# Performance work log

Measured on AMD Instinct MI355X. Metric: run time of the kernel, lower is better.

Reference implementation:

```python
import jax, jax.numpy as jnp
import numpy as np

N_NODES = 50000
K_EIG = 512
F_DIM = 128


def setup_inputs() -> dict:
    key = jax.random.key(0)
    k1, k2, k3 = jax.random.split(key, 3)
    eigenvectors = jax.random.normal(k1, (N_NODES, K_EIG), dtype=jnp.float32)
    spectral_filters = jax.random.normal(k2, (K_EIG,), dtype=jnp.float32)
    x = jax.random.normal(k3, (N_NODES, F_DIM), dtype=jnp.float32)
    return {"eigenvectors": eigenvectors, "spectral_filters": spectral_filters, "x": x}


def reference(eigenvectors, spectral_filters, x):
    # U @ diag(g) @ U.T @ x  ==  U @ (g[:, None] * (U.T @ x)); relu epilogue.
    spec = eigenvectors.T @ x                      # [k, f]
    logits = eigenvectors @ (spectral_filters[:, None] * spec)  # [n, f]
    return jax.nn.relu(logits)
```

## Files before the change

### kernel.cpp

```cpp
#include <hip/hip_runtime.h>
#include <hip/hip_bf16.h>

#define N_NODES 50000
#define K_EIG   512
#define F_DIM   128
#define NPAD    51200
#define NSPLITS 200
#define CHUNK   256
#define NT16    3136

typedef __attribute__((ext_vector_type(8))) short bf16x8;
typedef __attribute__((ext_vector_type(4))) short s16x4;
typedef __attribute__((ext_vector_type(4))) float f32x4;
typedef __attribute__((ext_vector_type(2))) unsigned u32x2;

static __device__ __forceinline__ unsigned pk2(float lo, float hi) {
    unsigned short a = __builtin_bit_cast(unsigned short, __float2bfloat16(lo));
    unsigned short b = __builtin_bit_cast(unsigned short, __float2bfloat16(hi));
    return ((unsigned)b << 16) | (unsigned)a;
}

static __device__ __forceinline__ short f2bf(float f) {
    union { float f; unsigned u; } v; v.f = f;
    unsigned r = v.u + 0x7fffu + ((v.u >> 16) & 1u);
    return (short)(r >> 16);
}

static __device__ __forceinline__ float bf2f(unsigned short u) {
    union { unsigned u; float f; } v; v.u = ((unsigned)u) << 16;
    return v.f;
}

__global__ __launch_bounds__(256) void prep_x(const float* __restrict__ x,
                                              unsigned short* __restrict__ xTa)
{
    const int n0 = blockIdx.x * 64;
    const int f0 = blockIdx.y * 64;
    const int fa = threadIdx.x & 15;
    const int nb = threadIdx.x >> 4;
    const int n  = n0 + 4 * nb;
    const int f  = f0 + 4 * fa;

    float r[4][4];
    #pragma unroll
    for (int jj = 0; jj < 4; ++jj) {
        int nr = n + jj;
        if (nr < N_NODES) {
            f32x4 v = *reinterpret_cast<const f32x4*>(x + (long)nr * F_DIM + f);
            r[jj][0] = v[0]; r[jj][1] = v[1]; r[jj][2] = v[2]; r[jj][3] = v[3];
        } else {
            r[jj][0] = r[jj][1] = r[jj][2] = r[jj][3] = 0.f;
        }
    }
    const int nt32 = n >> 5;
    const int hpart = ((n >> 3) & 3) * 16;
    const int slot  = 4 * (nb & 1);
    #pragma unroll
    for (int i = 0; i < 4; ++i) {
        int fi = f + i;
        size_t ad = ((size_t)((fi >> 4) * 1600 + nt32) * 64 + hpart + (fi & 15)) * 8 + slot;
        u32x2 w; w[0] = pk2(r[0][i], r[1][i]); w[1] = pk2(r[2][i], r[3][i]);
        *reinterpret_cast<u32x2*>(xTa + ad) = w;
    }
}

__global__ __launch_bounds__(256) void k_spec_f(
    const float* __restrict__ U, const unsigned short* __restrict__ xTa,
    unsigned short* __restrict__ Ubfa, unsigned short* __restrict__ part2)
{
    __shared__ unsigned char lds1[2][64 * 128];
    __shared__ unsigned char lds2[2][64 * 128];

    const int kt    = blockIdx.x;
    const int split = blockIdx.y;
    const int tid   = threadIdx.x;
    const int wid   = tid >> 6;
    const int lane  = tid & 63;
    const int h     = lane >> 4;
    const int m     = lane & 15;
    const int k0    = kt * 64;
    const int nbeg  = split * CHUNK;

    const int kq = tid & 15;
    const int nq = tid >> 4;

    f32x4 acc[4][2];
    #pragma unroll
    for (int s = 0; s < 4; ++s)
        #pragma unroll
        for (int t = 0; t < 2; ++t)
            #pragma unroll
            for (int e = 0; e < 4; ++e) acc[s][t][e] = 0.f;

    const unsigned short* Bl = xTa + (size_t)lane * 8;
    const int ftb = wid * 2;

    float  r[4][4];
    bf16x8 bfr[2][2];

    #pragma unroll
    for (int j = 0; j < 4; ++j) {
        int n = nbeg + 4 * nq + j;
        if (n < N_NODES) {
            f32x4 v = *reinterpret_cast<const f32x4*>(U + (long)n * K_EIG + k0 + 4 * kq);
            r[j][0] = v[0]; r[j][1] = v[1]; r[j][2] = v[2]; r[j][3] = v[3];
        } else {
            r[j][0] = r[j][1] = r[j][2] = r[j][3] = 0.f;
        }
    }
    #pragma unroll
    for (int sub = 0; sub < 2; ++sub)
        #pragma unroll
        for (int t = 0; t < 2; ++t)
            bfr[sub][t] = *reinterpret_cast<const bf16x8*>(
                Bl + (size_t)((ftb + t) * 1600 + (nbeg >> 5) + sub) * 512);

    #pragma unroll
    for (int step = 0; step < 4; ++step) {
        const int ntile = nbeg + 64 * step;
        const int buf   = step & 1;

        float  rN[4][4];
        bf16x8 bN[2][2];
        if (step < 3) {
            const int nt2 = ntile + 64;
            #pragma unroll
            for (int j = 0; j < 4; ++j) {
                int n = nt2 + 4 * nq + j;
                if (n < N_NODES) {
                    f32x4 v = *reinterpret_cast<const f32x4*>(
                        U + (long)n * K_EIG + k0 + 4 * kq);
                    rN[j][0] = v[0]; rN[j][1] = v[1]; rN[j][2] = v[2]; rN[j][3] = v[3];
                } else {
                    rN[j][0] = rN[j][1] = rN[j][2] = rN[j][3] = 0.f;
                }
            }
            #pragma unroll
            for (int sub = 0; sub < 2; ++sub)
                #pragma unroll
                for (int t = 0; t < 2; ++t)
                    bN[sub][t] = *reinterpret_cast<const bf16x8*>(
                        Bl + (size_t)((ftb + t) * 1600 + (nt2 >> 5) + sub) * 512);
        }

        #pragma unroll
        for (int i = 0; i < 4; ++i) {
            int kl = 4 * kq + i;
            unsigned lo = pk2(r[0][i], r[1][i]);
            unsigned hi = pk2(r[2][i], r[3][i]);
            int byte = (kl * 128 + 8 * nq) ^ ((kl & 7) << 4);
            *reinterpret_cast<unsigned long long*>(&lds1[buf][byte]) =
                ((unsigned long long)hi << 32) | (unsigned long long)lo;
        }
        #pragma unroll
        for (int j = 0; j < 4; ++j) {
            int nl = 4 * nq + j;
            unsigned lo = pk2(r[j][0], r[j][1]);
            unsigned hi = pk2(r[j][2], r[j][3]);
            int byte = (nl * 128 + 8 * kq) ^ ((nl & 7) << 4);
            *reinterpret_cast<unsigned long long*>(&lds2[buf][byte]) =
                ((unsigned long long)hi << 32) | (unsigned long long)lo;
        }
        __syncthreads();

        #pragma unroll
        for (int sub = 0; sub < 2; ++sub) {
            bf16x8 af[4];
            #pragma unroll
            for (int s = 0; s < 4; ++s) {
                int row  = 16 * s + m;
                int byte = (row * 128 + 64 * sub + 16 * h) ^ ((m & 7) << 4);
                af[s] = *reinterpret_cast<const bf16x8*>(&lds1[buf][byte]);
            }
            #pragma unroll
            for (int s = 0; s < 4; ++s)
                #pragma unroll
                for (int t = 0; t < 2; ++t)
                    acc[s][t] = __builtin_amdgcn_mfma_f32_16x16x32_bf16(
                        af[s], bfr[sub][t], acc[s][t], 0, 0, 0);
        }

        {
            const int fid = tid >> 5;
            const int q   = tid & 31;
            const int ntl = fid >> 1;
            const int ktl = fid & 1;
            if (ntile + ntl * 16 < N_NODES) {
                #pragma unroll
                for (int e = 0; e < 2; ++e) {
                    int l    = 2 * q + e;
                    int row  = ntl * 16 + (l & 15);
                    int byte = (row * 128 + ktl * 64 + 16 * (l >> 4)) ^ ((row & 7) << 4);
                    bf16x8 v = *reinterpret_cast<const bf16x8*>(&lds2[buf][byte]);
                    size_t ad = (((size_t)(ntile >> 4) + ntl) * 16 + (kt * 2 + ktl)) * 64 + l;
                    *reinterpret_cast<bf16x8*>(Ubfa + ad * 8) = v;
                }
            }
        }

        if (step < 3) {
            #pragma unroll
            for (int j = 0; j < 4; ++j)
                #pragma unroll
                for (int i = 0; i < 4; ++i) r[j][i] = rN[j][i];
            #pragma unroll
            for (int sub = 0; sub < 2; ++sub)
                #pragma unroll
                for (int t = 0; t < 2; ++t) bfr[sub][t] = bN[sub][t];
        }
    }

    unsigned short* pb = part2 + (((size_t)(kt * NSPLITS + split)) * 256 + tid) * 32;
    #pragma unroll
    for (int s = 0; s < 4; ++s) {
        bf16x8 v;
        #pragma unroll
        for (int e = 0; e < 4; ++e) {
            v[e]     = f2bf(acc[s][0][e]);
            v[e + 4] = f2bf(acc[s][1][e]);
        }
        *reinterpret_cast<bf16x8*>(pb + s * 8) = v;
    }
}

__global__ __launch_bounds__(256) void k_reduce1(
    const unsigned short* __restrict__ part2, float* __restrict__ part3)
{
    const int q  = blockIdx.x * 256 + threadIdx.x;
    const int pg = blockIdx.y;
    const int kt = q >> 11;
    const int tp = (q >> 3) & 255;
    const int sl = q & 7;
    f32x4 s; s[0] = s[1] = s[2] = s[3] = 0.f;
    const int pend = pg * 25 + 25;
    for (int p = pg * 25; p < pend; ++p) {
        s16x4 v = *reinterpret_cast<const s16x4*>(
            part2 + (((size_t)(kt * NSPLITS + p)) * 256 + tp) * 32 + sl * 4);
        s[0] += bf2f((unsigned short)v[0]); s[1] += bf2f((unsigned short)v[1]);
        s[2] += bf2f((unsigned short)v[2]); s[3] += bf2f((unsigned short)v[3]);
    }
    *reinterpret_cast<f32x4*>(part3 + ((size_t)pg * 16384 + q) * 4) = s;
}

__global__ __launch_bounds__(256) void k_reduce2(
    const float* __restrict__ part3, const float* __restrict__ g,
    unsigned short* __restrict__ specbfa)
{
    const int q = blockIdx.x * 256 + threadIdx.x;
    f32x4 s; s[0] = s[1] = s[2] = s[3] = 0.f;
    #pragma unroll
    for (int pg = 0; pg < 8; ++pg) {
        f32x4 v = *reinterpret_cast<const f32x4*>(part3 + ((size_t)pg * 16384 + q) * 4);
        s[0] += v[0]; s[1] += v[1]; s[2] += v[2]; s[3] += v[3];
    }
    const int kt = q >> 11, tp = (q >> 3) & 255, sl = q & 7;
    const int wid = tp >> 6, le = tp & 63, hh = le >> 4, mm = le & 15;
    const int ss = sl >> 1, tt = sl & 1;
    const int f = wid * 32 + tt * 16 + mm;
    const int k = kt * 64 + ss * 16 + hh * 4;
    f32x4 gv = *reinterpret_cast<const f32x4*>(g + k);
    s16x4 o;
    #pragma unroll
    for (int e = 0; e < 4; ++e) o[e] = f2bf(s[e] * gv[e]);
    const int lanep = ((k >> 3) & 3) * 16 + (f & 15);
    size_t ad = ((size_t)((f >> 4) * 16 + (k >> 5)) * 64 + lanep) * 8 + (k & 7);
    *reinterpret_cast<s16x4*>(specbfa + ad) = o;
}

__global__ __launch_bounds__(256) void k_out_bf(
    const unsigned short* __restrict__ Ubfa,
    const unsigned short* __restrict__ specbfa,
    float* __restrict__ out)
{
    const int tid  = threadIdx.x;
    const int wid  = tid >> 6;
    const int lane = tid & 63;
    const int h = lane >> 4, m = lane & 15;
    const int wr = wid >> 1, wc = wid & 1;
    const int nbase = blockIdx.x * 64 + wr * 32;
    const int fbase = wc * 64;

    const unsigned short* Al[2];
    #pragma unroll
    for (int i = 0; i < 2; ++i)
        Al[i] = Ubfa + ((size_t)((nbase >> 4) + i) * 8192 + lane * 8);
    const unsigned short* Blp[4];
    #pragma unroll
    for (int t = 0; t < 4; ++t)
        Blp[t] = specbfa + ((size_t)(4 * wc + t) * 8192 + lane * 8);

    f32x4 acc[2][4];
    #pragma unroll
    for (int i = 0; i < 2; ++i)
        #pragma unroll
        for (int t = 0; t < 4; ++t)
            #pragma unroll
            for (int e = 0; e < 4; ++e) acc[i][t][e] = 0.f;

    bf16x8 aC[2], bC[4];
    #pragma unroll
    for (int i = 0; i < 2; ++i) aC[i] = *reinterpret_cast<const bf16x8*>(Al[i]);
    #pragma unroll
    for (int t = 0; t < 4; ++t) bC[t] = *reinterpret_cast<const bf16x8*>(Blp[t]);

    for (int kb = 0; kb < 16; ++kb) {
        int kn = (kb + 1 < 16) ? kb + 1 : 0;
        bf16x8 aN[2], bN[4];
        #pragma unroll
        for (int i = 0; i < 2; ++i)
            aN[i] = *reinterpret_cast<const bf16x8*>(Al[i] + (size_t)kn * 512);
        #pragma unroll
        for (int t = 0; t < 4; ++t)
            bN[t] = *reinterpret_cast<const bf16x8*>(Blp[t] + (size_t)kn * 512);

        #pragma unroll
        for (int i = 0; i < 2; ++i)
            #pragma unroll
            for (int t = 0; t < 4; ++t)
                acc[i][t] = __builtin_amdgcn_mfma_f32_16x16x32_bf16(
                    aC[i], bC[t], acc[i][t], 0, 0, 0);

        #pragma unroll
        for (int i = 0; i < 2; ++i) aC[i] = aN[i];
        #pragma unroll
        for (int t = 0; t < 4; ++t) bC[t] = bN[t];
    }

    #pragma unroll
    for (int i = 0; i < 2; ++i)
        #pragma unroll
        for (int r = 0; r < 4; ++r) {
            int nn = nbase + 16 * i + 4 * h + r;
            if (nn < N_NODES) {
                float* orow = out + (long)nn * F_DIM + fbase + m;
                #pragma unroll
                for (int t = 0; t < 4; ++t)
                    orow[16 * t] = fmaxf(acc[i][t][r], 0.f);
            }
        }
}

__global__ __launch_bounds__(256) void k_spec_v1(
    const float* __restrict__ U, const float* __restrict__ g,
    const float* __restrict__ x, float* __restrict__ specT)
{
    const int kt    = blockIdx.x;
    const int split = blockIdx.y;
    const int tid   = threadIdx.x;
    const int wid   = tid >> 6;
    const int lane  = tid & 63;
    const int h     = lane >> 4;
    const int m     = lane & 15;
    const int k0 = kt * 64;
    const int f0 = wid * 32;
    const int chunk1 = 782;
    const int n_start = split * chunk1;
    int n_end = n_start + chunk1;
    if (n_end > N_NODES) n_end = N_NODES;

    f32x4 acc[4][2];
    #pragma unroll
    for (int s = 0; s < 4; ++s)
        #pragma unroll
        for (int t = 0; t < 2; ++t)
            #pragma unroll
            for (int e = 0; e < 4; ++e) acc[s][t][e] = 0.f;

    for (int nb = n_start; nb < n_end; nb += 32) {
        bf16x8 a[4]; bf16x8 b[2];
        const int nrow = nb + 8 * h;
        #pragma unroll
        for (int j = 0; j < 8; ++j) {
            int nn = nrow + j;
            bool valid = (nn < n_end);
            int nc = valid ? nn : (n_end - 1);
            const float* Urow = U + (long)nc * K_EIG + k0 + m;
            const float* Xrow = x + (long)nc * F_DIM + f0 + m;
            #pragma unroll
            for (int s = 0; s < 4; ++s) {
                short bv = f2bf(Urow[16 * s]);
                a[s][j] = valid ? bv : (short)0;
            }
            #pragma unroll
            for (int t = 0; t < 2; ++t) {
                short bv = f2bf(Xrow[16 * t]);
                b[t][j] = valid ? bv : (short)0;
            }
        }
        #pragma unroll
        for (int s = 0; s < 4; ++s)
            #pragma unroll
            for (int t = 0; t < 2; ++t)
                acc[s][t] = __builtin_amdgcn_mfma_f32_16x16x32_bf16(
                    a[s], b[t], acc[s][t], 0, 0, 0);
    }
    #pragma unroll
    for (int s = 0; s < 4; ++s)
        #pragma unroll
        for (int t = 0; t < 2; ++t)
            #pragma unroll
            for (int r = 0; r < 4; ++r) {
                int k = k0 + 16 * s + 4 * h + r;
                int f = f0 + 16 * t + m;
                atomicAdd(&specT[(long)f * K_EIG + k], acc[s][t][r] * g[k]);
            }
}

__global__ __launch_bounds__(256) void k_out_v1(
    const float* __restrict__ U, const float* __restrict__ specT,
    float* __restrict__ out)
{
    const int tid  = threadIdx.x;
    const int wid  = tid >> 6;
    const int lane = tid & 63;
    const int h = lane >> 4, m = lane & 15;
    const int wr = wid >> 1, wc = wid & 1;
    const int nbase = blockIdx.x * 128 + wr * 64;
    const int fbase = wc * 64;

    f32x4 acc[4][4];
    #pragma unroll
    for (int i = 0; i < 4; ++i)
        #pragma unroll
        for (int t = 0; t < 4; ++t)
            #pragma unroll
            for (int e = 0; e < 4; ++e) acc[i][t][e] = 0.f;

    for (int kb = 0; kb < K_EIG; kb += 32) {
        bf16x8 a[4], b[4];
        #pragma unroll
        for (int i = 0; i < 4; ++i) {
            int nn = nbase + 16 * i + m;
            bool valid = (nn < N_NODES);
            int nc = valid ? nn : (N_NODES - 1);
            const f32x4* p = reinterpret_cast<const f32x4*>(
                U + (long)nc * K_EIG + kb + 8 * h);
            f32x4 lo = p[0], hi = p[1];
            #pragma unroll
            for (int j = 0; j < 4; ++j) {
                short b0 = f2bf(lo[j]), b1 = f2bf(hi[j]);
                a[i][j]     = valid ? b0 : (short)0;
                a[i][j + 4] = valid ? b1 : (short)0;
            }
        }
        #pragma unroll
        for (int t = 0; t < 4; ++t) {
            const f32x4* p = reinterpret_cast<const f32x4*>(
                specT + (long)(fbase + 16 * t + m) * K_EIG + kb + 8 * h);
            f32x4 lo = p[0], hi = p[1];
            #pragma unroll
            for (int j = 0; j < 4; ++j) {
                b[t][j]     = f2bf(lo[j]);
                b[t][j + 4] = f2bf(hi[j]);
            }
        }
        #pragma unroll
        for (int i = 0; i < 4; ++i)
            #pragma unroll
            for (int t = 0; t < 4; ++t)
                acc[i][t] = __builtin_amdgcn_mfma_f32_16x16x32_bf16(
                    a[i], b[t], acc[i][t], 0, 0, 0);
    }
    #pragma unroll
    for (int i = 0; i < 4; ++i)
        #pragma unroll
        for (int r = 0; r < 4; ++r) {
            int nn = nbase + 16 * i + 4 * h + r;
            if (nn < N_NODES) {
                float* orow = out + (long)nn * F_DIM + fbase + m;
                #pragma unroll
                for (int t = 0; t < 4; ++t)
                    orow[16 * t] = fmaxf(acc[i][t][r], 0.f);
            }
        }
}

extern "C" void kernel_launch(void* const* d_in, const int* in_sizes, int n_in,
                              void* d_out, int out_size, void* d_ws, size_t ws_size,
                              hipStream_t stream) {
    const float* U = (const float*)d_in[0];
    const float* g = (const float*)d_in[1];
    const float* x = (const float*)d_in[2];
    float* out = (float*)d_out;

    const size_t OFF_XTA   = 0;
    const size_t OFF_PART  = 13107200;
    const size_t OFF_SPECA = 39321600;
    const size_t OFF_UBFA  = 39452672;
    const size_t OFF_PART3 = 90832896;
    const size_t WS_NEEDED = 92930048;

    if (ws_size >= WS_NEEDED) {
        unsigned short* xTa     = (unsigned short*)((char*)d_ws + OFF_XTA);
        unsigned short* part2   = (unsigned short*)((char*)d_ws + OFF_PART);
        unsigned short* specbfa = (unsigned short*)((char*)d_ws + OFF_SPECA);
        unsigned short* Ubfa    = (unsigned short*)((char*)d_ws + OFF_UBFA);
        float*          part3   = (float*)((char*)d_ws + OFF_PART3);

        dim3 gx(NPAD / 64, F_DIM / 64);
        prep_x<<<gx, 256, 0, stream>>>(x, xTa);

        dim3 g1(K_EIG / 64, NSPLITS);
        k_spec_f<<<g1, 256, 0, stream>>>(U, xTa, Ubfa, part2);

        dim3 gr1(64, 8);
        k_reduce1<<<gr1, 256, 0, stream>>>(part2, part3);
        k_reduce2<<<64, 256, 0, stream>>>(part3, g, specbfa);

        int nb2 = (N_NODES + 63) / 64;
        k_out_bf<<<nb2, 256, 0, stream>>>(Ubfa, specbfa, out);
    } else {
        float* specT = (float*)d_ws;
        hipMemsetAsync(specT, 0, (size_t)K_EIG * F_DIM * sizeof(float), stream);
        dim3 g1(K_EIG / 64, 64);
        k_spec_v1<<<g1, 256, 0, stream>>>(U, g, x, specT);
        int nb2 = (N_NODES + 127) / 128;
        k_out_v1<<<nb2, 256, 0, stream>>>(U, specT, out);
    }
}
```

Baseline: 95.27 us.

## Split U conversion into separate prep kernel and stream pre-swizzled bf16 tiles in spec GEMM

U is now converted to bf16 by its own kernel, prep_u, which writes two MFMA-ready layouts: a transposed UTa for the first GEMM and Ubfa for the output GEMM. The spec kernel then loads fragments straight from global memory with register double-buffering, so it no longer needs LDS staging or a barrier per step. The split count also changes from 200 to 160 chunks of 320 nodes. In exchange the code writes an extra 52 MB bf16 copy of U and launches one more kernel, and the workspace it needs grows to about 141 MB. If the workspace is smaller than that, the code silently falls back to the slow path.

```diff
diff --git a/kernel.cpp b/kernel.cpp
--- a/kernel.cpp
+++ b/kernel.cpp
@@ -5,9 +5,10 @@
 #define K_EIG   512
 #define F_DIM   128
 #define NPAD    51200
-#define NSPLITS 200
-#define CHUNK   256
-#define NT16    3136
+#define NSPLITS 160
+#define CHUNK   320
+#define NT32    1600
+#define NT16    3200
 
 typedef __attribute__((ext_vector_type(8))) short bf16x8;
 typedef __attribute__((ext_vector_type(4))) short s16x4;
@@ -58,49 +59,29 @@
     #pragma unroll
     for (int i = 0; i < 4; ++i) {
         int fi = f + i;
-        size_t ad = ((size_t)((fi >> 4) * 1600 + nt32) * 64 + hpart + (fi & 15)) * 8 + slot;
+        size_t ad = ((size_t)((fi >> 4) * NT32 + nt32) * 64 + hpart + (fi & 15)) * 8 + slot;
         u32x2 w; w[0] = pk2(r[0][i], r[1][i]); w[1] = pk2(r[2][i], r[3][i]);
         *reinterpret_cast<u32x2*>(xTa + ad) = w;
     }
 }
 
-__global__ __launch_bounds__(256) void k_spec_f(
-    const float* __restrict__ U, const unsigned short* __restrict__ xTa,
-    unsigned short* __restrict__ Ubfa, unsigned short* __restrict__ part2)
-{
-    __shared__ unsigned char lds1[2][64 * 128];
-    __shared__ unsigned char lds2[2][64 * 128];
-
-    const int kt    = blockIdx.x;
-    const int split = blockIdx.y;
-    const int tid   = threadIdx.x;
-    const int wid   = tid >> 6;
-    const int lane  = tid & 63;
-    const int h     = lane >> 4;
-    const int m     = lane & 15;
-    const int k0    = kt * 64;
-    const int nbeg  = split * CHUNK;
-
-    const int kq = tid & 15;
-    const int nq = tid >> 4;
-
-    f32x4 acc[4][2];
-    #pragma unroll
-    for (int s = 0; s < 4; ++s)
-        #pragma unroll
-        for (int t = 0; t < 2; ++t)
-            #pragma unroll
-            for (int e = 0; e < 4; ++e) acc[s][t][e] = 0.f;
-
-    const unsigned short* Bl = xTa + (size_t)lane * 8;
-    const int ftb = wid * 2;
-
-    float  r[4][4];
-    bf16x8 bfr[2][2];
-
+__global__ __launch_bounds__(256) void prep_u(const float* __restrict__ U,
+                                              unsigned short* __restrict__ UTa,
+                                              unsigned short* __restrict__ Ubfa)
+{
+    __shared__ unsigned char lds1[64 * 128];
+    __shared__ unsigned char lds2[64 * 128];
+
+    const int n0  = blockIdx.x * 64;
+    const int k0  = blockIdx.y * 64;
+    const int tid = threadIdx.x;
+    const int kq  = tid & 15;
+    const int nq  = tid >> 4;
+
+    float r[4][4];
     #pragma unroll
     for (int j = 0; j < 4; ++j) {
-        int n = nbeg + 4 * nq + j;
+        int n = n0 + 4 * nq + j;
         if (n < N_NODES) {
             f32x4 v = *reinterpret_cast<const f32x4*>(U + (long)n * K_EIG + k0 + 4 * kq);
             r[j][0] = v[0]; r[j][1] = v[1]; r[j][2] = v[2]; r[j][3] = v[3];
@@ -108,109 +89,112 @@
             r[j][0] = r[j][1] = r[j][2] = r[j][3] = 0.f;
         }
     }
-    #pragma unroll
-    for (int sub = 0; sub < 2; ++sub)
+
+    #pragma unroll
+    for (int i = 0; i < 4; ++i) {
+        int kl = 4 * kq + i;
+        unsigned lo = pk2(r[0][i], r[1][i]);
+        unsigned hi = pk2(r[2][i], r[3][i]);
+        int byte = (kl * 128 + 8 * nq) ^ ((kl & 7) << 4);
+        *reinterpret_cast<unsigned long long*>(lds1 + byte) =
+            ((unsigned long long)hi << 32) | (unsigned long long)lo;
+    }
+    #pragma unroll
+    for (int j = 0; j < 4; ++j) {
+        int nl = 4 * nq + j;
+        unsigned lo = pk2(r[j][0], r[j][1]);
+        unsigned hi = pk2(r[j][2], r[j][3]);
+        int byte = (nl * 128 + 8 * kq) ^ ((nl & 7) << 4);
+        *reinterpret_cast<unsigned long long*>(lds2 + byte) =
+            ((unsigned long long)hi << 32) | (unsigned long long)lo;
+    }
+    __syncthreads();
+
+    const int q = tid & 31;
+    {
+        const int fid = tid >> 5;
+        const int ntl = fid >> 1;
+        const int ktl = fid & 1;
+        #pragma unroll
+        for (int e = 0; e < 2; ++e) {
+            int l    = 2 * q + e;
+            int row  = ntl * 16 + (l & 15);
+            int byte = (row * 128 + ktl * 64 + 16 * (l >> 4)) ^ ((row & 7) << 4);
+            bf16x8 v = *reinterpret_cast<const bf16x8*>(lds2 + byte);
+            size_t ad = (((size_t)(n0 >> 4) + ntl) * 16 + ((k0 >> 5) + ktl)) * 64 + l;
+            *reinterpret_cast<bf16x8*>(Ubfa + ad * 8) = v;
+        }
+    }
+    {
+        const int fid = tid >> 5;
+        const int ktl = fid >> 1;
+        const int ntl = fid & 1;
+        #pragma unroll
+        for (int e = 0; e < 2; ++e) {
+            int l    = 2 * q + e;
+            int row  = ktl * 16 + (l & 15);
+            int byte = (row * 128 + ntl * 64 + 16 * (l >> 4)) ^ ((row & 7) << 4);
+            bf16x8 v = *reinterpret_cast<const bf16x8*>(lds1 + byte);
+            size_t ad = (((size_t)(k0 >> 4) + ktl) * NT32 + ((n0 >> 5) + ntl)) * 64 + l;
+            *reinterpret_cast<bf16x8*>(UTa + ad * 8) = v;
+        }
+    }
+}
+
+__global__ __launch_bounds__(256) void k_spec(
+    const unsigned short* __restrict__ UTa, const unsigned short* __restrict__ xTa,
+    unsigned short* __restrict__ part2)
+{
+    const int ktB   = blockIdx.x;
+    const int split = blockIdx.y;
+    const int tid   = threadIdx.x;
+    const int wid   = tid >> 6;
+    const int lane  = tid & 63;
+    const int nt0   = split * (CHUNK / 32);
+
+    f32x4 acc[4][2];
+    #pragma unroll
+    for (int s = 0; s < 4; ++s)
         #pragma unroll
         for (int t = 0; t < 2; ++t)
-            bfr[sub][t] = *reinterpret_cast<const bf16x8*>(
-                Bl + (size_t)((ftb + t) * 1600 + (nbeg >> 5) + sub) * 512);
-
-    #pragma unroll
-    for (int step = 0; step < 4; ++step) {
-        const int ntile = nbeg + 64 * step;
-        const int buf   = step & 1;
-
-        float  rN[4][4];
-        bf16x8 bN[2][2];
-        if (step < 3) {
-            const int nt2 = ntile + 64;
-            #pragma unroll
-            for (int j = 0; j < 4; ++j) {
-                int n = nt2 + 4 * nq + j;
-                if (n < N_NODES) {
-                    f32x4 v = *reinterpret_cast<const f32x4*>(
-                        U + (long)n * K_EIG + k0 + 4 * kq);
-                    rN[j][0] = v[0]; rN[j][1] = v[1]; rN[j][2] = v[2]; rN[j][3] = v[3];
-                } else {
-                    rN[j][0] = rN[j][1] = rN[j][2] = rN[j][3] = 0.f;
-                }
-            }
-            #pragma unroll
-            for (int sub = 0; sub < 2; ++sub)
-                #pragma unroll
-                for (int t = 0; t < 2; ++t)
-                    bN[sub][t] = *reinterpret_cast<const bf16x8*>(
-                        Bl + (size_t)((ftb + t) * 1600 + (nt2 >> 5) + sub) * 512);
-        }
-
-        #pragma unroll
-        for (int i = 0; i < 4; ++i) {
-            int kl = 4 * kq + i;
-            unsigned lo = pk2(r[0][i], r[1][i]);
-            unsigned hi = pk2(r[2][i], r[3][i]);
-            int byte = (kl * 128 + 8 * nq) ^ ((kl & 7) << 4);
-            *reinterpret_cast<unsigned long long*>(&lds1[buf][byte]) =
-                ((unsigned long long)hi << 32) | (unsigned long long)lo;
-        }
-        #pragma unroll
-        for (int j = 0; j < 4; ++j) {
-            int nl = 4 * nq + j;
-            unsigned lo = pk2(r[j][0], r[j][1]);
-            unsigned hi = pk2(r[j][2], r[j][3]);
-            int byte = (nl * 128 + 8 * kq) ^ ((nl & 7) << 4);
-            *reinterpret_cast<unsigned long long*>(&lds2[buf][byte]) =
-                ((unsigned long long)hi << 32) | (unsigned long long)lo;
-        }
-        __syncthreads();
-
-        #pragma unroll
-        for (int sub = 0; sub < 2; ++sub) {
-            bf16x8 af[4];
-            #pragma unroll
-            for (int s = 0; s < 4; ++s) {
-                int row  = 16 * s + m;
-                int byte = (row * 128 + 64 * sub + 16 * h) ^ ((m & 7) << 4);
-                af[s] = *reinterpret_cast<const bf16x8*>(&lds1[buf][byte]);
-            }
-            #pragma unroll
-            for (int s = 0; s < 4; ++s)
-                #pragma unroll
-                for (int t = 0; t < 2; ++t)
-                    acc[s][t] = __builtin_amdgcn_mfma_f32_16x16x32_bf16(
-                        af[s], bfr[sub][t], acc[s][t], 0, 0, 0);
-        }
-
-        {
-            const int fid = tid >> 5;
-            const int q   = tid & 31;
-            const int ntl = fid >> 1;
-            const int ktl = fid & 1;
-            if (ntile + ntl * 16 < N_NODES) {
-                #pragma unroll
-                for (int e = 0; e < 2; ++e) {
-                    int l    = 2 * q + e;
-                    int row  = ntl * 16 + (l & 15);
-                    int byte = (row * 128 + ktl * 64 + 16 * (l >> 4)) ^ ((row & 7) << 4);
-                    bf16x8 v = *reinterpret_cast<const bf16x8*>(&lds2[buf][byte]);
-                    size_t ad = (((size_t)(ntile >> 4) + ntl) * 16 + (kt * 2 + ktl)) * 64 + l;
-                    *reinterpret_cast<bf16x8*>(Ubfa + ad * 8) = v;
-                }
-            }
-        }
-
-        if (step < 3) {
-            #pragma unroll
-            for (int j = 0; j < 4; ++j)
-                #pragma unroll
-                for (int i = 0; i < 4; ++i) r[j][i] = rN[j][i];
-            #pragma unroll
-            for (int sub = 0; sub < 2; ++sub)
-                #pragma unroll
-                for (int t = 0; t < 2; ++t) bfr[sub][t] = bN[sub][t];
-        }
-    }
-
-    unsigned short* pb = part2 + (((size_t)(kt * NSPLITS + split)) * 256 + tid) * 32;
+            #pragma unroll
+            for (int e = 0; e < 4; ++e) acc[s][t][e] = 0.f;
+
+    const unsigned short* Abase = UTa + ((size_t)(ktB * 4) * NT32) * 512 + lane * 8;
+    const unsigned short* Bbase = xTa + ((size_t)(wid * 2) * NT32) * 512 + lane * 8;
+
+    bf16x8 aC[4], bC[2];
+    #pragma unroll
+    for (int s = 0; s < 4; ++s)
+        aC[s] = *reinterpret_cast<const bf16x8*>(Abase + ((size_t)s * NT32 + nt0) * 512);
+    #pragma unroll
+    for (int t = 0; t < 2; ++t)
+        bC[t] = *reinterpret_cast<const bf16x8*>(Bbase + ((size_t)t * NT32 + nt0) * 512);
+
+    for (int step = 0; step < CHUNK / 32; ++step) {
+        int ntn = nt0 + ((step + 1 < CHUNK / 32) ? step + 1 : 0);
+        bf16x8 aN[4], bN[2];
+        #pragma unroll
+        for (int s = 0; s < 4; ++s)
+            aN[s] = *reinterpret_cast<const bf16x8*>(Abase + ((size_t)s * NT32 + ntn) * 512);
+        #pragma unroll
+        for (int t = 0; t < 2; ++t)
+            bN[t] = *reinterpret_cast<const bf16x8*>(Bbase + ((size_t)t * NT32 + ntn) * 512);
+
+        #pragma unroll
+        for (int s = 0; s < 4; ++s)
+            #pragma unroll
+            for (int t = 0; t < 2; ++t)
+                acc[s][t] = __builtin_amdgcn_mfma_f32_16x16x32_bf16(
+                    aC[s], bC[t], acc[s][t], 0, 0, 0);
+
+        #pragma unroll
+        for (int s = 0; s < 4; ++s) aC[s] = aN[s];
+        #pragma unroll
+        for (int t = 0; t < 2; ++t) bC[t] = bN[t];
+    }
+
+    unsigned short* pb = part2 + (((size_t)(ktB * NSPLITS + split)) * 256 + tid) * 32;
     #pragma unroll
     for (int s = 0; s < 4; ++s) {
         bf16x8 v;
@@ -232,8 +216,8 @@
     const int tp = (q >> 3) & 255;
     const int sl = q & 7;
     f32x4 s; s[0] = s[1] = s[2] = s[3] = 0.f;
-    const int pend = pg * 25 + 25;
-    for (int p = pg * 25; p < pend; ++p) {
+    const int pend = pg * 20 + 20;
+    for (int p = pg * 20; p < pend; ++p) {
         s16x4 v = *reinterpret_cast<const s16x4*>(
             part2 + (((size_t)(kt * NSPLITS + p)) * 256 + tp) * 32 + sl * 4);
         s[0] += bf2f((unsigned short)v[0]); s[1] += bf2f((unsigned short)v[1]);
@@ -484,24 +468,29 @@
     float* out = (float*)d_out;
 
     const size_t OFF_XTA   = 0;
-    const size_t OFF_PART  = 13107200;
-    const size_t OFF_SPECA = 39321600;
-    const size_t OFF_UBFA  = 39452672;
-    const size_t OFF_PART3 = 90832896;
-    const size_t WS_NEEDED = 92930048;
+    const size_t OFF_UTA   = 13107200;
+    const size_t OFF_UBFA  = 65536000;
+    const size_t OFF_PART2 = 117964800;
+    const size_t OFF_PART3 = 138936320;
+    const size_t OFF_SPECA = 141033472;
+    const size_t WS_NEEDED = 141164544;
 
     if (ws_size >= WS_NEEDED) {
         unsigned short* xTa     = (unsigned short*)((char*)d_ws + OFF_XTA);
-        unsigned short* part2   = (unsigned short*)((char*)d_ws + OFF_PART);
+        unsigned short* UTa     = (unsigned short*)((char*)d_ws + OFF_UTA);
+        unsigned short* Ubfa    = (unsigned short*)((char*)d_ws + OFF_UBFA);
+        unsigned short* part2   = (unsigned short*)((char*)d_ws + OFF_PART2);
+        float*          part3   = (float*)((char*)d_ws + OFF_PART3);
         unsigned short* specbfa = (unsigned short*)((char*)d_ws + OFF_SPECA);
-        unsigned short* Ubfa    = (unsigned short*)((char*)d_ws + OFF_UBFA);
-        float*          part3   = (float*)((char*)d_ws + OFF_PART3);
 
         dim3 gx(NPAD / 64, F_DIM / 64);
         prep_x<<<gx, 256, 0, stream>>>(x, xTa);
 
+        dim3 gu(NPAD / 64, K_EIG / 64);
+        prep_u<<<gu, 256, 0, stream>>>(U, UTa, Ubfa);
+
         dim3 g1(K_EIG / 64, NSPLITS);
-        k_spec_f<<<g1, 256, 0, stream>>>(U, xTa, Ubfa, part2);
+        k_spec<<<g1, 256, 0, stream>>>(UTa, xTa, part2);
 
         dim3 gr1(64, 8);
         k_reduce1<<<gr1, 256, 0, stream>>>(part2, part3);
```

Result: slower. 107.1 us (+12.5%).

## Drop bf16 eigenvector staging; read fp32 U directly in output GEMM

Applied to the files above, without the earlier changes.

The first GEMM no longer writes a bf16 copy of U (Ubfa) through a second LDS transpose buffer. The output GEMM now loads fp32 rows of U directly and converts them to bf16 in registers before each MFMA. This removes a ~51MB write and a 51MB read of the bf16 copy, at the cost of reading 102MB of fp32 U in the second pass and doing conversion ALU work there. The spec-kernel grid order is also swapped so the split index is blockIdx.x.

```diff
diff --git a/kernel.cpp b/kernel.cpp
--- a/kernel.cpp
+++ b/kernel.cpp
@@ -7,7 +7,7 @@
 #define NPAD    51200
 #define NSPLITS 200
 #define CHUNK   256
-#define NT16    3136
+#define NT32    1600
 
 typedef __attribute__((ext_vector_type(8))) short bf16x8;
 typedef __attribute__((ext_vector_type(4))) short s16x4;
@@ -58,7 +58,7 @@
     #pragma unroll
     for (int i = 0; i < 4; ++i) {
         int fi = f + i;
-        size_t ad = ((size_t)((fi >> 4) * 1600 + nt32) * 64 + hpart + (fi & 15)) * 8 + slot;
+        size_t ad = ((size_t)((fi >> 4) * NT32 + nt32) * 64 + hpart + (fi & 15)) * 8 + slot;
         u32x2 w; w[0] = pk2(r[0][i], r[1][i]); w[1] = pk2(r[2][i], r[3][i]);
         *reinterpret_cast<u32x2*>(xTa + ad) = w;
     }
@@ -66,13 +66,12 @@
 
 __global__ __launch_bounds__(256) void k_spec_f(
     const float* __restrict__ U, const unsigned short* __restrict__ xTa,
-    unsigned short* __restrict__ Ubfa, unsigned short* __restrict__ part2)
+    unsigned short* __restrict__ part2)
 {
     __shared__ unsigned char lds1[2][64 * 128];
-    __shared__ unsigned char lds2[2][64 * 128];
-
-    const int kt    = blockIdx.x;
-    const int split = blockIdx.y;
+
+    const int split = blockIdx.x;
+    const int kt    = blockIdx.y;
     const int tid   = threadIdx.x;
     const int wid   = tid >> 6;
     const int lane  = tid & 63;
@@ -113,7 +112,7 @@
         #pragma unroll
         for (int t = 0; t < 2; ++t)
             bfr[sub][t] = *reinterpret_cast<const bf16x8*>(
-                Bl + (size_t)((ftb + t) * 1600 + (nbeg >> 5) + sub) * 512);
+                Bl + (size_t)((ftb + t) * NT32 + (nbeg >> 5) + sub) * 512);
 
     #pragma unroll
     for (int step = 0; step < 4; ++step) {
@@ -140,7 +139,7 @@
                 #pragma unroll
                 for (int t = 0; t < 2; ++t)
                     bN[sub][t] = *reinterpret_cast<const bf16x8*>(
-                        Bl + (size_t)((ftb + t) * 1600 + (nt2 >> 5) + sub) * 512);
+                        Bl + (size_t)((ftb + t) * NT32 + (nt2 >> 5) + sub) * 512);
         }
 
         #pragma unroll
@@ -152,15 +151,6 @@
             *reinterpret_cast<unsigned long long*>(&lds1[buf][byte]) =
                 ((unsigned long long)hi << 32) | (unsigned long long)lo;
         }
-        #pragma unroll
-        for (int j = 0; j < 4; ++j) {
-            int nl = 4 * nq + j;
-            unsigned lo = pk2(r[j][0], r[j][1]);
-            unsigned hi = pk2(r[j][2], r[j][3]);
-            int byte = (nl * 128 + 8 * kq) ^ ((nl & 7) << 4);
-            *reinterpret_cast<unsigned long long*>(&lds2[buf][byte]) =
-                ((unsigned long long)hi << 32) | (unsigned long long)lo;
-        }
         __syncthreads();
 
         #pragma unroll
@@ -178,24 +168,6 @@
                 for (int t = 0; t < 2; ++t)
                     acc[s][t] = __builtin_amdgcn_mfma_f32_16x16x32_bf16(
                         af[s], bfr[sub][t], acc[s][t], 0, 0, 0);
-        }
-
-        {
-            const int fid = tid >> 5;
-            const int q   = tid & 31;
-            const int ntl = fid >> 1;
-            const int ktl = fid & 1;
-            if (ntile + ntl * 16 < N_NODES) {
-                #pragma unroll
-                for (int e = 0; e < 2; ++e) {
-                    int l    = 2 * q + e;
-                    int row  = ntl * 16 + (l & 15);
-                    int byte = (row * 128 + ktl * 64 + 16 * (l >> 4)) ^ ((row & 7) << 4);
-                    bf16x8 v = *reinterpret_cast<const bf16x8*>(&lds2[buf][byte]);
-                    size_t ad = (((size_t)(ntile >> 4) + ntl) * 16 + (kt * 2 + ktl)) * 64 + l;
-                    *reinterpret_cast<bf16x8*>(Ubfa + ad * 8) = v;
-                }
-            }
         }
 
         if (step < 3) {
@@ -267,9 +239,8 @@
     *reinterpret_cast<s16x4*>(specbfa + ad) = o;
 }
 
-__global__ __launch_bounds__(256) void k_out_bf(
-    const unsigned short* __restrict__ Ubfa,
-    const unsigned short* __restrict__ specbfa,
+__global__ __launch_bounds__(256) void k_out_f32(
+    const float* __restrict__ U, const unsigned short* __restrict__ specbfa,
     float* __restrict__ out)
 {
     const int tid  = threadIdx.x;
@@ -280,10 +251,13 @@
     const int nbase = blockIdx.x * 64 + wr * 32;
     const int fbase = wc * 64;
 
-    const unsigned short* Al[2];
-    #pragma unroll
-    for (int i = 0; i < 2; ++i)
-        Al[i] = Ubfa + ((size_t)((nbase >> 4) + i) * 8192 + lane * 8);
+    const float* Arow[2];
+    #pragma unroll
+    for (int i = 0; i < 2; ++i) {
+        int n  = nbase + 16 * i + m;
+        int nc = (n < N_NODES) ? n : (N_NODES - 1);
+        Arow[i] = U + (size_t)nc * K_EIG + 8 * h;
+    }
     const unsigned short* Blp[4];
     #pragma unroll
     for (int t = 0; t < 4; ++t)
@@ -297,31 +271,45 @@
             #pragma unroll
             for (int e = 0; e < 4; ++e) acc[i][t][e] = 0.f;
 
-    bf16x8 aC[2], bC[4];
-    #pragma unroll
-    for (int i = 0; i < 2; ++i) aC[i] = *reinterpret_cast<const bf16x8*>(Al[i]);
-    #pragma unroll
-    for (int t = 0; t < 4; ++t) bC[t] = *reinterpret_cast<const bf16x8*>(Blp[t]);
+    f32x4 loC[2], hiC[2]; bf16x8 bC[4];
+    #pragma unroll
+    for (int i = 0; i < 2; ++i) {
+        loC[i] = *reinterpret_cast<const f32x4*>(Arow[i]);
+        hiC[i] = *reinterpret_cast<const f32x4*>(Arow[i] + 4);
+    }
+    #pragma unroll
+    for (int t = 0; t < 4; ++t)
+        bC[t] = *reinterpret_cast<const bf16x8*>(Blp[t]);
 
     for (int kb = 0; kb < 16; ++kb) {
         int kn = (kb + 1 < 16) ? kb + 1 : 0;
-        bf16x8 aN[2], bN[4];
-        #pragma unroll
-        for (int i = 0; i < 2; ++i)
-            aN[i] = *reinterpret_cast<const bf16x8*>(Al[i] + (size_t)kn * 512);
+        f32x4 loN[2], hiN[2]; bf16x8 bN[4];
+        #pragma unroll
+        for (int i = 0; i < 2; ++i) {
+            loN[i] = *reinterpret_cast<const f32x4*>(Arow[i] + kn * 32);
+            hiN[i] = *reinterpret_cast<const f32x4*>(Arow[i] + kn * 32 + 4);
+        }
         #pragma unroll
         for (int t = 0; t < 4; ++t)
             bN[t] = *reinterpret_cast<const bf16x8*>(Blp[t] + (size_t)kn * 512);
 
+        bf16x8 a[2];
+        #pragma unroll
+        for (int i = 0; i < 2; ++i)
+            #pragma unroll
+            for (int j = 0; j < 4; ++j) {
+                a[i][j]     = f2bf(loC[i][j]);
+                a[i][j + 4] = f2bf(hiC[i][j]);
+            }
         #pragma unroll
         for (int i = 0; i < 2; ++i)
             #pragma unroll
             for (int t = 0; t < 4; ++t)
                 acc[i][t] = __builtin_amdgcn_mfma_f32_16x16x32_bf16(
-                    aC[i], bC[t], acc[i][t], 0, 0, 0);
-
-        #pragma unroll
-        for (int i = 0; i < 2; ++i) aC[i] = aN[i];
+                    a[i], bC[t], acc[i][t], 0, 0, 0);
+
+        #pragma unroll
+        for (int i = 0; i < 2; ++i) { loC[i] = loN[i]; hiC[i] = hiN[i]; }
         #pragma unroll
         for (int t = 0; t < 4; ++t) bC[t] = bN[t];
     }
@@ -484,31 +472,29 @@
     float* out = (float*)d_out;
 
     const size_t OFF_XTA   = 0;
-    const size_t OFF_PART  = 13107200;
-    const size_t OFF_SPECA = 39321600;
-    const size_t OFF_UBFA  = 39452672;
-    const size_t OFF_PART3 = 90832896;
-    const size_t WS_NEEDED = 92930048;
+    const size_t OFF_PART2 = 13107200;
+    const size_t OFF_PART3 = 39321600;
+    const size_t OFF_SPECA = 41418752;
+    const size_t WS_NEEDED = 41549824;
 
     if (ws_size >= WS_NEEDED) {
         unsigned short* xTa     = (unsigned short*)((char*)d_ws + OFF_XTA);
-        unsigned short* part2   = (unsigned short*)((char*)d_ws + OFF_PART);
+        unsigned short* part2   = (unsigned short*)((char*)d_ws + OFF_PART2);
+        float*          part3   = (float*)((char*)d_ws + OFF_PART3);
         unsigned short* specbfa = (unsigned short*)((char*)d_ws + OFF_SPECA);
-        unsigned short* Ubfa    = (unsigned short*)((char*)d_ws + OFF_UBFA);
-        float*          part3   = (float*)((char*)d_ws + OFF_PART3);
 
         dim3 gx(NPAD / 64, F_DIM / 64);
         prep_x<<<gx, 256, 0, stream>>>(x, xTa);
 
-        dim3 g1(K_EIG / 64, NSPLITS);
-        k_spec_f<<<g1, 256, 0, stream>>>(U, xTa, Ubfa, part2);
+        dim3 g1(NSPLITS, K_EIG / 64);
+        k_spec_f<<<g1, 256, 0, stream>>>(U, xTa, part2);
 
         dim3 gr1(64, 8);
         k_reduce1<<<gr1, 256, 0, stream>>>(part2, part3);
         k_reduce2<<<64, 256, 0, stream>>>(part3, g, specbfa);
 
         int nb2 = (N_NODES + 63) / 64;
-        k_out_bf<<<nb2, 256, 0, stream>>>(Ubfa, specbfa, out);
+        k_out_f32<<<nb2, 256, 0, stream>>>(U, specbfa, out);
     } else {
         float* specT = (float*)d_ws;
         hipMemsetAsync(specT, 0, (size_t)K_EIG * F_DIM * sizeof(float), stream);
```

Measured after the change: 96.86 us. No clear change (+1.7%).
